# Kernel optimization log

Measured on AMD Instinct MI355X. Metric: run time of the kernel, lower is better.

## Reference

```python
import jax, jax.numpy as jnp
import numpy as np

B, CQ, CKV, H, W = 8, 256, 512, 64, 64
HKV, WKV = 32, 32
DQK = CQ // 8  # 32


def setup_inputs() -> dict:
    key = jax.random.key(0)
    ks = jax.random.split(key, 9)
    s = 0.05
    return {
        "query": jax.random.normal(ks[0], (B, CQ, H, W), jnp.float32),
        "key_value": jax.random.normal(ks[1], (B, CKV, HKV, WKV), jnp.float32),
        "Wq": jax.random.normal(ks[2], (DQK, CQ), jnp.float32) * s,
        "bq": jax.random.normal(ks[3], (DQK,), jnp.float32) * s,
        "Wk": jax.random.normal(ks[4], (DQK, CKV), jnp.float32) * s,
        "bk": jax.random.normal(ks[5], (DQK,), jnp.float32) * s,
        "Wv": jax.random.normal(ks[6], (CQ, CKV), jnp.float32) * s,
        "bv": jax.random.normal(ks[7], (CQ,), jnp.float32) * s,
        "gamma": jax.random.normal(ks[8], (1,), jnp.float32) * 0.5,
    }


def reference(query, key_value, Wq, bq, Wk, bk, Wv, bv, gamma):
    b, cq, h, w = query.shape
    n = h * w
    # bilinear resize of key_value to query's spatial size (align_corners=False
    # half-pixel convention, matching torch F.interpolate and jax.image.resize)
    kv = jax.image.resize(key_value, (b, key_value.shape[1], h, w), method="bilinear")
    # 1x1 convs are channel contractions
    q = jnp.einsum("bchw,dc->bdhw", query, Wq) + bq[None, :, None, None]   # [B,DQK,H,W]
    k = jnp.einsum("bchw,dc->bdhw", kv, Wk) + bk[None, :, None, None]      # [B,DQK,H,W]
    v = jnp.einsum("bchw,dc->bdhw", kv, Wv) + bv[None, :, None, None]      # [B,CQ,H,W]
    qf = q.reshape(b, -1, n)   # [B,DQK,N]
    kf = k.reshape(b, -1, n)   # [B,DQK,N]
    vf = v.reshape(b, -1, n)   # [B,CQ,N]
    energy = jnp.einsum("bdn,bdm->bnm", qf, kf)        # [B,N,N]
    attention = jax.nn.softmax(energy, axis=-1)
    out = jnp.einsum("bnm,bcm->bcn", attention, vf)     # [B,CQ,N]
    out = out.reshape(b, cq, h, w)
    return gamma[0] * out + query
```

## Files before the change

### kernel.cpp

```cpp
#include <hip/hip_runtime.h>

#define B_ 8
#define CQ_ 256
#define CKV_ 512
#define N_ 4096
#define DQK_ 32
#define LOG2E 1.44269504f

typedef __bf16 bf16;
typedef __bf16 bf16x4 __attribute__((ext_vector_type(4)));
typedef __bf16 bf16x8 __attribute__((ext_vector_type(8)));
typedef float f32x4 __attribute__((ext_vector_type(4)));

__global__ void k_convert_w(const float* __restrict__ Wq, const float* __restrict__ Wk,
                            const float* __restrict__ Wv,
                            bf16* __restrict__ wq, bf16* __restrict__ wk, bf16* __restrict__ wv) {
    int i = blockIdx.x * 256 + threadIdx.x;
    if (i < 8192) wq[i] = (bf16)(Wq[i] * LOG2E);
    else if (i < 24576) wk[i - 8192] = (bf16)Wk[i - 8192];
    else if (i < 155648) wv[i - 24576] = (bf16)Wv[i - 24576];
}

__global__ __launch_bounds__(256) void k_resize(const float* __restrict__ kv, bf16* __restrict__ kvr) {
    const int yo = blockIdx.x;
    const int b  = blockIdx.y;
    const int uc = blockIdx.z * 64;
    const int tid = threadIdx.x;
    __shared__ float r0[64][33];
    __shared__ float r1[64][33];
    int ty = yo >> 1;
    int y0, y1; float wy0, wy1;
    if ((yo & 1) == 0) { y0 = ty > 0 ? ty - 1 : 0; y1 = ty; wy0 = 0.25f; wy1 = 0.75f; }
    else               { y0 = ty; y1 = ty < 31 ? ty + 1 : 31; wy0 = 0.75f; wy1 = 0.25f; }
    const int u_loc = tid & 63;
    const int xo_base = tid >> 6;
    for (int i = 0; i < 8; ++i) {
        int idx = tid + i * 256;
        int u = idx >> 5, x = idx & 31;
        const float* src = kv + ((size_t)b * CKV_ + uc + u) * 1024 + x;
        r0[u][x] = src[y0 * 32];
        r1[u][x] = src[y1 * 32];
    }
    __syncthreads();
    for (int i = 0; i < 16; ++i) {
        int xo = xo_base + i * 4;
        int tx = xo >> 1;
        int xa, xb; float wxa, wxb;
        if ((xo & 1) == 0) { xa = tx > 0 ? tx - 1 : 0; xb = tx; wxa = 0.25f; wxb = 0.75f; }
        else               { xa = tx; xb = tx < 31 ? tx + 1 : 31; wxa = 0.75f; wxb = 0.25f; }
        float v0 = wxa * r0[u_loc][xa] + wxb * r0[u_loc][xb];
        float v1 = wxa * r1[u_loc][xa] + wxb * r1[u_loc][xb];
        float val = wy0 * v0 + wy1 * v1;
        kvr[((size_t)b * N_ + yo * 64 + xo) * CKV_ + uc + u_loc] = (bf16)val;
    }
}

__global__ __launch_bounds__(256) void k_proj_q_fused(const float* __restrict__ query,
                                                      const bf16* __restrict__ W,
                                                      const float* __restrict__ bias,
                                                      bf16* __restrict__ qTb) {
    __shared__ bf16 tile[64][264];
    const int n0 = blockIdx.x * 64;
    const int b  = blockIdx.y;
    const int tid = threadIdx.x;
    const int xi = tid & 15, c0 = tid >> 4;
    for (int pass = 0; pass < 16; ++pass) {
        int c = c0 + pass * 16;
        const float4 v = *(const float4*)(query + ((size_t)b * CQ_ + c) * N_ + n0 + xi * 4);
        tile[xi * 4 + 0][c] = (bf16)v.x;
        tile[xi * 4 + 1][c] = (bf16)v.y;
        tile[xi * 4 + 2][c] = (bf16)v.z;
        tile[xi * 4 + 3][c] = (bf16)v.w;
    }
    __syncthreads();
    const int w = tid >> 6, lane = tid & 63;
    const int l16 = lane & 15, quad = lane >> 4;
    const int ct = w & 1, nh = w >> 1;
    f32x4 acc[2];
    acc[0] = (f32x4){0.f, 0.f, 0.f, 0.f}; acc[1] = (f32x4){0.f, 0.f, 0.f, 0.f};
    const bf16* aptr = W + (ct * 16 + l16) * CQ_ + quad * 8;
#pragma unroll
    for (int ks = 0; ks < 8; ++ks) {
        bf16x8 af = *(const bf16x8*)(aptr + ks * 32);
        for (int j = 0; j < 2; ++j) {
            bf16x8 bfv = *(const bf16x8*)&tile[nh * 32 + j * 16 + l16][ks * 32 + quad * 8];
            acc[j] = __builtin_amdgcn_mfma_f32_16x16x32_bf16(af, bfv, acc[j], 0, 0, 0);
        }
    }
    for (int j = 0; j < 2; ++j)
        for (int r = 0; r < 4; ++r) {
            int d = ct * 16 + quad * 4 + r;
            int n = n0 + nh * 32 + j * 16 + l16;
            qTb[((size_t)b * N_ + n) * DQK_ + d] = (bf16)(acc[j][r] + bias[d] * LOG2E);
        }
}

__global__ __launch_bounds__(256) void k_proj_k(const bf16* __restrict__ W,
                                                const float* __restrict__ bias,
                                                const bf16* __restrict__ Bm,
                                                bf16* __restrict__ outT) {
    const int flat = blockIdx.x + 128 * blockIdx.y;
    const int b  = flat & 7;
    const int mb = (flat >> 3) * 32;
    const int tid = threadIdx.x;
    const int w = tid >> 6, lane = tid & 63;
    const int l16 = lane & 15, quad = lane >> 4;
    const int ct = w & 1;
    const int mh = (w >> 1) * 16;
    f32x4 acc = (f32x4){0.f, 0.f, 0.f, 0.f};
    const bf16* aptr = W + (ct * 16 + l16) * CKV_ + quad * 8;
    const bf16* bptr = Bm + ((size_t)b * N_ + mb + mh + l16) * CKV_ + quad * 8;
#pragma unroll
    for (int ks = 0; ks < 16; ++ks) {
        bf16x8 af  = *(const bf16x8*)(aptr + ks * 32);
        bf16x8 bfv = *(const bf16x8*)(bptr + ks * 32);
        acc = __builtin_amdgcn_mfma_f32_16x16x32_bf16(af, bfv, acc, 0, 0, 0);
    }
    const int m = mb + mh + l16;
    for (int r = 0; r < 4; ++r) {
        int d = ct * 16 + quad * 4 + r;
        outT[((size_t)b * N_ + m) * DQK_ + d] = (bf16)(acc[r] + bias[d]);
    }
}

__global__ __launch_bounds__(256) void k_proj_v(const bf16* __restrict__ W,
                                                const float* __restrict__ bias,
                                                const bf16* __restrict__ Bm,
                                                bf16* __restrict__ vout) {
    const int flat = blockIdx.x + 128 * blockIdx.y;
    const int b  = flat & 7;
    const int mb = (flat >> 3) * 32;
    const int tid = threadIdx.x;
    const int w = tid >> 6, lane = tid & 63;
    const int l16 = lane & 15, quad = lane >> 4;
    f32x4 acc[4][2];
    for (int i = 0; i < 4; ++i) for (int j = 0; j < 2; ++j) acc[i][j] = (f32x4){0.f, 0.f, 0.f, 0.f};
    const bf16* bbase = Bm + ((size_t)b * N_ + mb) * CKV_ + quad * 8;
#pragma unroll 4
    for (int ks = 0; ks < 16; ++ks) {
        bf16x8 bfv[2];
        for (int j = 0; j < 2; ++j)
            bfv[j] = *(const bf16x8*)(bbase + (size_t)(j * 16 + l16) * CKV_ + ks * 32);
        for (int i = 0; i < 4; ++i) {
            bf16x8 af = *(const bf16x8*)(W + (size_t)((w * 4 + i) * 16 + l16) * CKV_ + ks * 32 + quad * 8);
            for (int j = 0; j < 2; ++j)
                acc[i][j] = __builtin_amdgcn_mfma_f32_16x16x32_bf16(af, bfv[j], acc[i][j], 0, 0, 0);
        }
    }
    for (int i = 0; i < 4; ++i)
        for (int r = 0; r < 4; ++r) {
            int c = (w * 4 + i) * 16 + quad * 4 + r;
            float bvs = bias[c];
            for (int j = 0; j < 2; ++j) {
                int m = mb + j * 16 + l16;
                vout[((size_t)b * CQ_ + c) * N_ + m] = (bf16)(acc[i][j][r] + bvs);
            }
        }
}

__global__ __launch_bounds__(256) void k_flash(const bf16* __restrict__ qT,
                                               const bf16* __restrict__ kT,
                                               const bf16* __restrict__ vv,
                                               float* __restrict__ o0,
                                               float* __restrict__ o1,
                                               float* __restrict__ ls0,
                                               float* __restrict__ ls1) {
    __shared__ bf16 P[2][64][72];
    const int z = blockIdx.z;
    const int tid = threadIdx.x;
    const int w = tid >> 6, lane = tid & 63;
    const int l16 = lane & 15, quad = lane >> 4;
    const int swz = l16 & 3;
    const int flat = blockIdx.x + 64 * blockIdx.y;
    const int b  = flat & 7;
    const int n0 = (flat >> 3) * 64;

    const bf16x8 qfrag = *(const bf16x8*)(qT + ((size_t)b * N_ + n0 + w * 16 + l16) * DQK_ + quad * 8);

    f32x4 acc[4][4];
    for (int i = 0; i < 4; ++i) for (int j = 0; j < 4; ++j) acc[i][j] = (f32x4){0.f, 0.f, 0.f, 0.f};
    f32x4 lsum = (f32x4){0.f, 0.f, 0.f, 0.f};

    const bf16* kbase = kT + (size_t)b * N_ * DQK_;
    const bf16* vbase = vv + ((size_t)b * CQ_ + w * 64) * N_;

    auto loadK = [&](int mt, bf16x8* dst) {
        for (int im = 0; im < 4; ++im)
            dst[im] = *(const bf16x8*)(kbase + (size_t)(mt * 64 + im * 16 + l16) * DQK_ + quad * 8);
    };
    auto computeS = [&](const bf16x8* kfr, bf16 (*Pb)[72]) {
        for (int im = 0; im < 4; ++im) {
            f32x4 s = __builtin_amdgcn_mfma_f32_16x16x32_bf16(kfr[im], qfrag,
                                                              (f32x4){0.f, 0.f, 0.f, 0.f}, 0, 0, 0);
            bf16x4 pk;
            for (int r = 0; r < 4; ++r) {
                float p = exp2f(s[r]);
                lsum[r] += p;
                pk[r] = (bf16)p;
            }
            *(bf16x4*)&Pb[w * 16 + l16][((im ^ swz) << 4) + quad * 4] = pk;
        }
    };
    bf16x8 kf[4];
    loadK(z, kf);
    computeS(kf, P[0]);
    loadK(2 + z, kf);
    __syncthreads();

    for (int u = 0; u < 31; ++u) {
        const int m0 = (2 * u + z) * 64;
        bf16x8 vf[2][4];
        for (int ks = 0; ks < 2; ++ks)
            for (int i = 0; i < 4; ++i)
                vf[ks][i] = *(const bf16x8*)(vbase + (size_t)(i * 16 + l16) * N_ + m0 + ks * 32 + quad * 8);
        bf16x8 kn[4];
        loadK(u + 2 < 32 ? 2 * (u + 2) + z : z, kn);
        computeS(kf, P[(u + 1) & 1]);
        bf16 (* __restrict__ Pb)[72] = P[u & 1];
        __builtin_amdgcn_s_setprio(1);
        for (int ks = 0; ks < 2; ++ks) {
            bf16x8 pf[4];
            for (int j = 0; j < 4; ++j)
                pf[j] = *(const bf16x8*)&Pb[j * 16 + l16]
                            [((((ks << 1) | (quad >> 1)) ^ swz) << 4) + ((quad & 1) << 3)];
            for (int i = 0; i < 4; ++i)
                for (int j = 0; j < 4; ++j)
                    acc[i][j] = __builtin_amdgcn_mfma_f32_16x16x32_bf16(vf[ks][i], pf[j], acc[i][j], 0, 0, 0);
        }
        __builtin_amdgcn_s_setprio(0);
        for (int im = 0; im < 4; ++im) kf[im] = kn[im];
        __syncthreads();
    }
    {
        const int m0 = (62 + z) * 64;
        bf16x8 vf[2][4];
        for (int ks = 0; ks < 2; ++ks)
            for (int i = 0; i < 4; ++i)
                vf[ks][i] = *(const bf16x8*)(vbase + (size_t)(i * 16 + l16) * N_ + m0 + ks * 32 + quad * 8);
        bf16 (* __restrict__ Pb)[72] = P[1];
        for (int ks = 0; ks < 2; ++ks) {
            bf16x8 pf[4];
            for (int j = 0; j < 4; ++j)
                pf[j] = *(const bf16x8*)&Pb[j * 16 + l16]
                            [((((ks << 1) | (quad >> 1)) ^ swz) << 4) + ((quad & 1) << 3)];
            for (int i = 0; i < 4; ++i)
                for (int j = 0; j < 4; ++j)
                    acc[i][j] = __builtin_amdgcn_mfma_f32_16x16x32_bf16(vf[ks][i], pf[j], acc[i][j], 0, 0, 0);
        }
    }
    float s = (lsum[0] + lsum[1]) + (lsum[2] + lsum[3]);
    s += __shfl_xor(s, 16);
    s += __shfl_xor(s, 32);
    float* lsz = z ? ls1 : ls0;
    if (quad == 0) lsz[(size_t)b * N_ + n0 + w * 16 + l16] = s;
    float* oz = z ? o1 : o0;
    for (int i = 0; i < 4; ++i)
        for (int r = 0; r < 4; ++r) {
            int c = w * 64 + i * 16 + quad * 4 + r;
            for (int j = 0; j < 4; ++j) {
                int n = n0 + j * 16 + l16;
                oz[((size_t)b * CQ_ + c) * N_ + n] = acc[i][j][r];
            }
        }
}

__global__ __launch_bounds__(256) void k_combine(const float* __restrict__ o1,
                                                 const float* __restrict__ ls0,
                                                 const float* __restrict__ ls1,
                                                 const float* __restrict__ query,
                                                 const float* __restrict__ gamma,
                                                 float* __restrict__ out) {
    const float g = gamma[0];
    const size_t total = (size_t)B_ * CQ_ * (N_ / 4);
    for (size_t i = (size_t)blockIdx.x * 256 + threadIdx.x; i < total; i += (size_t)gridDim.x * 256) {
        size_t n4 = i & (N_ / 4 - 1);
        size_t b  = i >> 18;
        float4 a0 = ((const float4*)out)[i];
        float4 a1 = ((const float4*)o1)[i];
        float4 l0 = *(const float4*)&ls0[b * N_ + n4 * 4];
        float4 l1 = *(const float4*)&ls1[b * N_ + n4 * 4];
        float4 q  = ((const float4*)query)[i];
        float4 r;
        r.x = g * (a0.x + a1.x) / (l0.x + l1.x) + q.x;
        r.y = g * (a0.y + a1.y) / (l0.y + l1.y) + q.y;
        r.z = g * (a0.z + a1.z) / (l0.z + l1.z) + q.z;
        r.w = g * (a0.w + a1.w) / (l0.w + l1.w) + q.w;
        ((float4*)out)[i] = r;
    }
}

extern "C" void kernel_launch(void* const* d_in, const int* in_sizes, int n_in,
                              void* d_out, int out_size, void* d_ws, size_t ws_size,
                              hipStream_t stream) {
    const float* query     = (const float*)d_in[0];
    const float* key_value = (const float*)d_in[1];
    const float* Wq = (const float*)d_in[2];
    const float* bq = (const float*)d_in[3];
    const float* Wk = (const float*)d_in[4];
    const float* bk = (const float*)d_in[5];
    const float* Wv = (const float*)d_in[6];
    const float* bv = (const float*)d_in[7];
    const float* gamma = (const float*)d_in[8];
    float* out = (float*)d_out;

    char* ws = (char*)d_ws;
    bf16* kvr  = (bf16*)(ws);
    bf16* vbuf = (bf16*)(ws + 33554432);
    bf16* qTb  = (bf16*)(ws + 50331648);
    bf16* kTb  = (bf16*)(ws + 52428800);
    bf16* wqb  = (bf16*)(ws + 54525952);
    bf16* wkb  = (bf16*)(ws + 54542336);
    bf16* wvb  = (bf16*)(ws + 54575104);
    float* ls0 = (float*)(ws + 54837248);
    float* ls1 = (float*)(ws + 54968320);

    k_convert_w<<<608, 256, 0, stream>>>(Wq, Wk, Wv, wqb, wkb, wvb);
    k_resize<<<dim3(64, 8, 8), 256, 0, stream>>>(key_value, kvr);
    k_proj_q_fused<<<dim3(64, 8), 256, 0, stream>>>(query, wqb, bq, qTb);
    k_proj_k<<<dim3(128, 8), 256, 0, stream>>>(wkb, bk, kvr, kTb);
    k_proj_v<<<dim3(128, 8), 256, 0, stream>>>(wvb, bv, kvr, vbuf);
    k_flash<<<dim3(64, 8, 2), 256, 0, stream>>>(qTb, kTb, vbuf, out, (float*)kvr, ls0, ls1);
    k_combine<<<2048, 256, 0, stream>>>((float*)kvr, ls0, ls1, query, gamma, out);
}
```

Measured before the change: 360.4 us.

## Split flash attention over value channels instead of keys, fuse epilogue

The flash kernel's z-split moves from halves of the key sequence to halves of the 256 value channels. Each block now walks all 64 key tiles and keeps half the accumulators, so it can normalise by its own row sum and apply gamma plus the residual in place. This removes the separate combine kernel and the fp32 partial-output and row-sum round trips through global memory. In exchange both z-halves recompute the QK^T scores and exponentials, doubling that work, and a launch_bounds occupancy hint of 4 is added.

```diff
diff --git a/kernel.cpp b/kernel.cpp
--- a/kernel.cpp
+++ b/kernel.cpp
@@ -158,14 +158,14 @@
         }
 }
 
-__global__ __launch_bounds__(256) void k_flash(const bf16* __restrict__ qT,
-                                               const bf16* __restrict__ kT,
-                                               const bf16* __restrict__ vv,
-                                               float* __restrict__ o0,
-                                               float* __restrict__ o1,
-                                               float* __restrict__ ls0,
-                                               float* __restrict__ ls1) {
+__global__ __launch_bounds__(256, 4) void k_flash(const bf16* __restrict__ qT,
+                                                  const bf16* __restrict__ kT,
+                                                  const bf16* __restrict__ vv,
+                                                  const float* __restrict__ query,
+                                                  const float* __restrict__ gamma,
+                                                  float* __restrict__ out) {
     __shared__ bf16 P[2][64][72];
+    __shared__ float linvs[64];
     const int z = blockIdx.z;
     const int tid = threadIdx.x;
     const int w = tid >> 6, lane = tid & 63;
@@ -177,12 +177,12 @@
 
     const bf16x8 qfrag = *(const bf16x8*)(qT + ((size_t)b * N_ + n0 + w * 16 + l16) * DQK_ + quad * 8);
 
-    f32x4 acc[4][4];
-    for (int i = 0; i < 4; ++i) for (int j = 0; j < 4; ++j) acc[i][j] = (f32x4){0.f, 0.f, 0.f, 0.f};
+    f32x4 acc[2][4];
+    for (int i = 0; i < 2; ++i) for (int j = 0; j < 4; ++j) acc[i][j] = (f32x4){0.f, 0.f, 0.f, 0.f};
     f32x4 lsum = (f32x4){0.f, 0.f, 0.f, 0.f};
 
     const bf16* kbase = kT + (size_t)b * N_ * DQK_;
-    const bf16* vbase = vv + ((size_t)b * CQ_ + w * 64) * N_;
+    const bf16* vbase = vv + ((size_t)b * CQ_ + z * 128 + w * 32) * N_;
 
     auto loadK = [&](int mt, bf16x8* dst) {
         for (int im = 0; im < 4; ++im)
@@ -201,21 +201,21 @@
             *(bf16x4*)&Pb[w * 16 + l16][((im ^ swz) << 4) + quad * 4] = pk;
         }
     };
+
     bf16x8 kf[4];
-    loadK(z, kf);
+    loadK(0, kf);
     computeS(kf, P[0]);
-    loadK(2 + z, kf);
-    __syncthreads();
-
-    for (int u = 0; u < 31; ++u) {
-        const int m0 = (2 * u + z) * 64;
-        bf16x8 vf[2][4];
+    loadK(1, kf);
+    __syncthreads();
+
+    for (int u = 0; u < 63; ++u) {
+        const int m0 = u * 64;
+        bf16x8 vf[2][2];
         for (int ks = 0; ks < 2; ++ks)
-            for (int i = 0; i < 4; ++i)
+            for (int i = 0; i < 2; ++i)
                 vf[ks][i] = *(const bf16x8*)(vbase + (size_t)(i * 16 + l16) * N_ + m0 + ks * 32 + quad * 8);
-        bf16x8 kn[4];
-        loadK(u + 2 < 32 ? 2 * (u + 2) + z : z, kn);
         computeS(kf, P[(u + 1) & 1]);
+        loadK(u + 2 < 64 ? u + 2 : 0, kf);
         bf16 (* __restrict__ Pb)[72] = P[u & 1];
         __builtin_amdgcn_s_setprio(1);
         for (int ks = 0; ks < 2; ++ks) {
@@ -223,19 +223,18 @@
             for (int j = 0; j < 4; ++j)
                 pf[j] = *(const bf16x8*)&Pb[j * 16 + l16]
                             [((((ks << 1) | (quad >> 1)) ^ swz) << 4) + ((quad & 1) << 3)];
-            for (int i = 0; i < 4; ++i)
+            for (int i = 0; i < 2; ++i)
                 for (int j = 0; j < 4; ++j)
                     acc[i][j] = __builtin_amdgcn_mfma_f32_16x16x32_bf16(vf[ks][i], pf[j], acc[i][j], 0, 0, 0);
         }
         __builtin_amdgcn_s_setprio(0);
-        for (int im = 0; im < 4; ++im) kf[im] = kn[im];
         __syncthreads();
     }
     {
-        const int m0 = (62 + z) * 64;
-        bf16x8 vf[2][4];
+        const int m0 = 63 * 64;
+        bf16x8 vf[2][2];
         for (int ks = 0; ks < 2; ++ks)
-            for (int i = 0; i < 4; ++i)
+            for (int i = 0; i < 2; ++i)
                 vf[ks][i] = *(const bf16x8*)(vbase + (size_t)(i * 16 + l16) * N_ + m0 + ks * 32 + quad * 8);
         bf16 (* __restrict__ Pb)[72] = P[1];
         for (int ks = 0; ks < 2; ++ks) {
@@ -243,7 +242,7 @@
             for (int j = 0; j < 4; ++j)
                 pf[j] = *(const bf16x8*)&Pb[j * 16 + l16]
                             [((((ks << 1) | (quad >> 1)) ^ swz) << 4) + ((quad & 1) << 3)];
-            for (int i = 0; i < 4; ++i)
+            for (int i = 0; i < 2; ++i)
                 for (int j = 0; j < 4; ++j)
                     acc[i][j] = __builtin_amdgcn_mfma_f32_16x16x32_bf16(vf[ks][i], pf[j], acc[i][j], 0, 0, 0);
         }
@@ -251,42 +250,20 @@
     float s = (lsum[0] + lsum[1]) + (lsum[2] + lsum[3]);
     s += __shfl_xor(s, 16);
     s += __shfl_xor(s, 32);
-    float* lsz = z ? ls1 : ls0;
-    if (quad == 0) lsz[(size_t)b * N_ + n0 + w * 16 + l16] = s;
-    float* oz = z ? o1 : o0;
-    for (int i = 0; i < 4; ++i)
+    if (lane < 16) linvs[w * 16 + l16] = 1.f / s;
+    __syncthreads();
+    float linv[4];
+    for (int j = 0; j < 4; ++j) linv[j] = linvs[j * 16 + l16];
+    const float g = gamma[0];
+    for (int i = 0; i < 2; ++i)
         for (int r = 0; r < 4; ++r) {
-            int c = w * 64 + i * 16 + quad * 4 + r;
+            int c = z * 128 + w * 32 + i * 16 + quad * 4 + r;
             for (int j = 0; j < 4; ++j) {
                 int n = n0 + j * 16 + l16;
-                oz[((size_t)b * CQ_ + c) * N_ + n] = acc[i][j][r];
+                size_t idx = ((size_t)b * CQ_ + c) * N_ + n;
+                out[idx] = g * acc[i][j][r] * linv[j] + query[idx];
             }
         }
-}
-
-__global__ __launch_bounds__(256) void k_combine(const float* __restrict__ o1,
-                                                 const float* __restrict__ ls0,
-                                                 const float* __restrict__ ls1,
-                                                 const float* __restrict__ query,
-                                                 const float* __restrict__ gamma,
-                                                 float* __restrict__ out) {
-    const float g = gamma[0];
-    const size_t total = (size_t)B_ * CQ_ * (N_ / 4);
-    for (size_t i = (size_t)blockIdx.x * 256 + threadIdx.x; i < total; i += (size_t)gridDim.x * 256) {
-        size_t n4 = i & (N_ / 4 - 1);
-        size_t b  = i >> 18;
-        float4 a0 = ((const float4*)out)[i];
-        float4 a1 = ((const float4*)o1)[i];
-        float4 l0 = *(const float4*)&ls0[b * N_ + n4 * 4];
-        float4 l1 = *(const float4*)&ls1[b * N_ + n4 * 4];
-        float4 q  = ((const float4*)query)[i];
-        float4 r;
-        r.x = g * (a0.x + a1.x) / (l0.x + l1.x) + q.x;
-        r.y = g * (a0.y + a1.y) / (l0.y + l1.y) + q.y;
-        r.z = g * (a0.z + a1.z) / (l0.z + l1.z) + q.z;
-        r.w = g * (a0.w + a1.w) / (l0.w + l1.w) + q.w;
-        ((float4*)out)[i] = r;
-    }
 }
 
 extern "C" void kernel_launch(void* const* d_in, const int* in_sizes, int n_in,
@@ -311,14 +288,11 @@
     bf16* wqb  = (bf16*)(ws + 54525952);
     bf16* wkb  = (bf16*)(ws + 54542336);
     bf16* wvb  = (bf16*)(ws + 54575104);
-    float* ls0 = (float*)(ws + 54837248);
-    float* ls1 = (float*)(ws + 54968320);
 
     k_convert_w<<<608, 256, 0, stream>>>(Wq, Wk, Wv, wqb, wkb, wvb);
     k_resize<<<dim3(64, 8, 8), 256, 0, stream>>>(key_value, kvr);
     k_proj_q_fused<<<dim3(64, 8), 256, 0, stream>>>(query, wqb, bq, qTb);
     k_proj_k<<<dim3(128, 8), 256, 0, stream>>>(wkb, bk, kvr, kTb);
     k_proj_v<<<dim3(128, 8), 256, 0, stream>>>(wvb, bv, kvr, vbuf);
-    k_flash<<<dim3(64, 8, 2), 256, 0, stream>>>(qTb, kTb, vbuf, out, (float*)kvr, ls0, ls1);
-    k_combine<<<2048, 256, 0, stream>>>((float*)kvr, ls0, ls1, query, gamma, out);
-}
+    k_flash<<<dim3(64, 8, 2), 256, 0, stream>>>(qTb, kTb, vbuf, query, gamma, out);
+}
```

Result: no change. 358.6 us (-0.5%).
